# Performance work log

Measured on AMD Instinct MI355X. Metric: run time of the kernel, lower is better.

Reference implementation:

```python
import jax, jax.numpy as jnp
import numpy as np
from jax import lax

EPS = 1e-5
F_CH = 32  # TIM future channels = int(256/8)
B_CH = 32  # TIM past channels (note: source bug -> these are zeroed, not shifted)


def inorm(x):
    # InstanceNorm3d (no affine): normalize each (b, c) over (T, H, W), biased var
    m = jnp.mean(x, axis=(2, 3, 4), keepdims=True)
    v = jnp.var(x, axis=(2, 3, 4), keepdims=True)
    return (x - m) * lax.rsqrt(v + EPS)


def conv1x1(x, w):
    # pointwise conv: x [B,C,T,H,W], w [O,C]
    return jnp.einsum('bcthw,oc->bothw', x, w)


def dwconv(x, w, pad):
    # depthwise 3D conv; w [C,1,kd,kh,kw], pad = [(pd,pd),(ph,ph),(pw,pw)]
    return lax.conv_general_dilated(
        x, w, window_strides=(1, 1, 1), padding=pad,
        feature_group_count=x.shape[1],
        dimension_numbers=('NCDHW', 'OIDHW', 'NCDHW'))


def tim(x):
    # Non-circular temporal interlacing. Faithful to source (past slice is a no-op):
    # channels [0:f]  <- x shifted from future (t+1), zero-padded at last frame
    # channels [f:f+b] <- zeros
    # channels [f+b:] <- identity
    f, b = F_CH, B_CH
    fut = jnp.concatenate([x[:, :f, 1:], jnp.zeros_like(x[:, :f, :1])], axis=2)
    mid = jnp.zeros_like(x[:, f:f + b])
    return jnp.concatenate([fut, mid, x[:, f + b:]], axis=1)


def setup_inputs() -> dict:
    key = jax.random.key(0)
    ks = jax.random.split(key, 7)
    cin, hid, cout = 64, 256, 64
    x = jax.random.normal(ks[0], (4, cin, 16, 64, 64), dtype=jnp.float32)
    w1 = jax.random.normal(ks[1], (hid, cin), dtype=jnp.float32) * 0.05
    w_dw_s = jax.random.normal(ks[2], (hid, 1, 1, 3, 3), dtype=jnp.float32) * 0.1
    w_dw_t = jax.random.normal(ks[3], (hid, 1, 3, 1, 1), dtype=jnp.float32) * 0.1
    w_se1 = jax.random.normal(ks[4], (hid // 4, hid), dtype=jnp.float32) * 0.05
    w_se2 = jax.random.normal(ks[5], (hid, hid // 4), dtype=jnp.float32) * 0.05
    w_proj = jax.random.normal(ks[6], (cout, hid), dtype=jnp.float32) * 0.05
    return {'x': x, 'w1': w1, 'w_dw_s': w_dw_s, 'w_dw_t': w_dw_t,
            'w_se1': w_se1, 'w_se2': w_se2, 'w_proj': w_proj}


def reference(x, w1, w_dw_s, w_dw_t, w_se1, w_se2, w_proj):
    shortcut = x
    # stage1: expand 1x1 conv + IN + ReLU
    h = jax.nn.relu(inorm(conv1x1(x, w1)))
    # temporal interlace (zero-FLOP channel shift)
    h = tim(h)
    # stage2: depthwise spatial (1,3,3) + IN + ReLU
    h = jax.nn.relu(inorm(dwconv(h, w_dw_s, [(0, 0), (1, 1), (1, 1)])))
    # stage3: depthwise temporal (3,1,1) + IN + ReLU
    h = jax.nn.relu(inorm(dwconv(h, w_dw_t, [(1, 1), (0, 0), (0, 0)])))
    # squeeze-excite
    y = jnp.mean(h, axis=(2, 3, 4), keepdims=True)           # [B,C,1,1,1]
    y = jax.nn.relu(jnp.einsum('bcthw,oc->bothw', y, w_se1))
    y = jax.nn.sigmoid(jnp.einsum('bcthw,oc->bothw', y, w_se2))
    h = h * y
    # proj 1x1 + IN, residual, maxpool (1,2,2)
    out = inorm(conv1x1(h, w_proj)) + shortcut
    out = lax.reduce_window(out, -jnp.inf, lax.max,
                            (1, 1, 1, 2, 2), (1, 1, 1, 2, 2), 'VALID')
    return out
```

## Files before the change

kernel.cpp:

```cpp
#include <hip/hip_runtime.h>
#include <hip/hip_bf16.h>

#define B_   4
#define CIN  64
#define HID  256
#define COUT 64
#define T_   16
#define H_   64
#define W_   64
#define HW_  (H_*W_)
#define THW  (T_*HW_)
#define EPS  1e-5f

typedef unsigned short ushort_t;
typedef unsigned int   uint_t;
typedef short bf16x8 __attribute__((ext_vector_type(8)));
typedef float f32x4  __attribute__((ext_vector_type(4)));

#define SA1   0
#define SB1   1024
#define SM3   4096
#define SIS3  5120
#define SSES  6144
#define SAL   7168
#define SBE   8192
__device__ float g_stats[10240];
__device__ float g_eps [4*1024*256];
__device__ float g_epss[4*1024*256];
__device__ ushort_t g_wpack[32768];

__device__ __forceinline__ float bf2f(ushort_t u) {
    return __uint_as_float(((uint_t)u) << 16);
}
__device__ __forceinline__ ushort_t f2bf(float f) {
    uint_t u = __float_as_uint(f);
    uint_t r = u + 0x7fffu + ((u >> 16) & 1u);
    return (ushort_t)(r >> 16);
}
__device__ __forceinline__ void unpacknorm2(uint2 k, float a, float bb, float* v) {
    uint_t uu[2] = {k.x, k.y};
    #pragma unroll
    for (int j = 0; j < 2; ++j) {
        v[2*j]   = fmaxf(fmaf(__uint_as_float(uu[j] << 16),         a, bb), 0.f);
        v[2*j+1] = fmaxf(fmaf(__uint_as_float(uu[j] & 0xffff0000u), a, bb), 0.f);
    }
}

__global__ __launch_bounds__(256) void k_prep(const float* __restrict__ w1,
                                              const float* __restrict__ wproj) {
    int idx = blockIdx.x*256 + threadIdx.x;
    {
        int j = idx & 7, lane = (idx>>3) & 63, ot = (idx>>9) & 3;
        int ks = (idx>>11) & 1, wv = idx >> 12;
        int ln = lane & 15, q = lane >> 4;
        int o = wv*64 + ot*16 + ln, k = ks*32 + q*8 + j;
        g_wpack[idx] = f2bf(w1[o*CIN + k]);
    }
    {
        int j = idx & 7, lane = (idx>>3) & 63, ot = (idx>>9) & 3, kg = idx >> 11;
        int ln = lane & 15, q = lane >> 4;
        int o = ot*16 + ln, k = kg*32 + q*8 + j;
        g_wpack[16384 + idx] = f2bf(wproj[o*HID + k]);
    }
}

__global__ __launch_bounds__(256) void k_expand(const float* __restrict__ x,
                                                ushort_t* __restrict__ h1, int b0) {
    union SMem {
        ushort_t Bs[64*72];
        float    red[2][256][16];
    };
    __shared__ SMem sm;
    const int tid = threadIdx.x;
    const int bb  = blockIdx.y, gb = b0 + bb;
    const int pos0 = blockIdx.x * 64;
    const int lane = tid & 63, wv = tid >> 6;
    const int q = lane >> 4, ln = lane & 15;

    bf16x8 af[2][4];
    #pragma unroll
    for (int ks = 0; ks < 2; ++ks)
        #pragma unroll
        for (int ot = 0; ot < 4; ++ot)
            af[ks][ot] = *(const bf16x8*)&g_wpack[(((wv*2+ks)*4+ot)<<9) + lane*8];

    #pragma unroll
    for (int i = 0; i < 4; ++i) {
        int lin = i*1024 + tid*4;
        int k = lin >> 6, n0 = lin & 63;
        float4 v = *(const float4*)&x[(size_t)(gb*CIN + k) * THW + pos0 + n0];
        ushort_t* d = &sm.Bs[k*72 + ((n0 + 16*((k>>3)&3)) & 63)];
        d[0] = f2bf(v.x); d[1] = f2bf(v.y); d[2] = f2bf(v.z); d[3] = f2bf(v.w);
    }
    __syncthreads();

    f32x4 acc[4][4];
    #pragma unroll
    for (int i = 0; i < 4; ++i)
        #pragma unroll
        for (int j = 0; j < 4; ++j)
            acc[i][j] = (f32x4){0.f,0.f,0.f,0.f};

    #pragma unroll
    for (int ks = 0; ks < 2; ++ks) {
        bf16x8 bfr[4];
        #pragma unroll
        for (int nt = 0; nt < 4; ++nt) {
            union { short s[8]; bf16x8 v; } bu;
            #pragma unroll
            for (int j = 0; j < 8; ++j) {
                int k = ks*32 + q*8 + j;
                int nn = (nt*16 + ln + 16*((k>>3)&3)) & 63;
                bu.s[j] = (short)sm.Bs[k*72 + nn];
            }
            bfr[nt] = bu.v;
        }
        #pragma unroll
        for (int ot = 0; ot < 4; ++ot)
            #pragma unroll
            for (int nt = 0; nt < 4; ++nt)
                acc[ot][nt] = __builtin_amdgcn_mfma_f32_16x16x32_bf16(
                    af[ks][ot], bfr[nt], acc[ot][nt], 0, 0, 0);
    }

    float sp_[16], ssp_[16];
    #pragma unroll
    for (int i = 0; i < 16; ++i) { sp_[i] = 0.f; ssp_[i] = 0.f; }

    #pragma unroll
    for (int ot = 0; ot < 4; ++ot)
        #pragma unroll
        for (int nt = 0; nt < 4; ++nt)
            #pragma unroll
            for (int r = 0; r < 4; ++r) {
                float vv = acc[ot][nt][r];
                int o = wv*64 + ot*16 + q*4 + r;
                int n = nt*16 + ln;
                h1[((size_t)bb*HID + o)*THW + pos0 + n] = f2bf(vv);
                sp_[ot*4+r] += vv;
                ssp_[ot*4+r] = fmaf(vv, vv, ssp_[ot*4+r]);
            }

    __syncthreads();
    #pragma unroll
    for (int i = 0; i < 16; ++i) {
        int o = wv*64 + (i>>2)*16 + q*4 + (i&3);
        sm.red[0][o][ln] = sp_[i];
        sm.red[1][o][ln] = ssp_[i];
    }
    __syncthreads();
    {
        float s = 0.f, ss = 0.f;
        #pragma unroll
        for (int l = 0; l < 16; ++l) {
            s  += sm.red[0][tid][l];
            ss += sm.red[1][tid][l];
        }
        size_t base = ((size_t)bb*1024 + blockIdx.x)*256 + tid;
        g_eps [base] = s;
        g_epss[base] = ss;
    }
}

__global__ __launch_bounds__(256) void k_red() {
    const int tid = threadIdx.x;
    const int cg  = blockIdx.x;
    const int bb  = blockIdx.y;
    const int ch  = cg*16 + (tid & 15);
    const int pb0 = tid >> 4;
    const float* ps  = &g_eps [((size_t)bb*1024)*256];
    const float* pss = &g_epss[((size_t)bb*1024)*256];
    float s = 0.f, ss = 0.f;
    #pragma unroll 8
    for (int it = 0; it < 64; ++it) {
        int pb = it*16 + pb0;
        s  += ps [(size_t)pb*256 + ch];
        ss += pss[(size_t)pb*256 + ch];
    }
    __shared__ float rs[256], rss[256];
    rs[tid] = s; rss[tid] = ss;
    __syncthreads();
    if (tid < 16) {
        float st = 0.f, sst = 0.f;
        #pragma unroll
        for (int k = 0; k < 16; ++k) { st += rs[tid + 16*k]; sst += rss[tid + 16*k]; }
        float m = st * (1.f/THW);
        float v = sst * (1.f/THW) - m*m;
        float is = 1.f / sqrtf(v + EPS);
        int ch_ = cg*16 + tid;
        int bc = bb*HID + ch_;
        g_stats[SA1 + bc] = is;
        g_stats[SB1 + bc] = -m * is;
        if (ch_ >= 32 && ch_ < 64) {
            g_stats[SM3  + bc] = 0.f;
            g_stats[SIS3 + bc] = 1.f / sqrtf(EPS);
            g_stats[SSES + bc] = 0.f;
        }
    }
}

__global__ __launch_bounds__(1024) void k_mid(const ushort_t* __restrict__ h1,
                                              const float* __restrict__ wdws,
                                              const float* __restrict__ wdwt,
                                              ushort_t* __restrict__ h3) {
    const int tid = threadIdx.x;
    const int oc  = blockIdx.x;
    const int o   = (oc < 32) ? oc : oc + 32;
    const int bb  = blockIdx.y;
    const int bc  = bb*HID + o;
    const int wid = tid >> 6, lane = tid & 63;

    __shared__ float pl[4][66*67];
    __shared__ float ls[16], lss[16];
    __shared__ float sa, sb;

    const float a1 = g_stats[SA1 + bc];
    const float b1 = g_stats[SB1 + bc];

    if (tid < 66) {
        #pragma unroll
        for (int b = 0; b < 4; ++b) {
            pl[b][tid]         = 0.f;
            pl[b][65*67 + tid] = 0.f;
            pl[b][tid*67]      = 0.f;
            pl[b][tid*67 + 65] = 0.f;
        }
    }

    const int fut = (o < 32) ? 1 : 0;
    const int y   = tid >> 4;
    const int x0  = (tid & 15) * 4;
    const ushort_t* chp = h1 + (size_t)bc * THW;
    const int lastp = fut ? (T_-2) : (T_-1);

    float wf[9];
    #pragma unroll
    for (int k = 0; k < 9; ++k) wf[k] = wdws[o*9 + k];

    uint2 sreg[4];
    sreg[0] = *(const uint2*)(chp + (size_t)(0+fut)*HW_ + tid*4);
    sreg[1] = *(const uint2*)(chp + (size_t)(1+fut)*HW_ + tid*4);
    #pragma unroll
    for (int p = 0; p < 2; ++p) {
        float vv[4];
        unpacknorm2(sreg[p], a1, b1, vv);
        float* dst = &pl[p][(y+1)*67 + x0 + 1];
        #pragma unroll
        for (int i = 0; i < 4; ++i) dst[i] = vv[i];
    }
    sreg[2] = *(const uint2*)(chp + (size_t)(2+fut)*HW_ + tid*4);
    sreg[3] = *(const uint2*)(chp + (size_t)(3+fut)*HW_ + tid*4);
    __syncthreads();

    uint2 keep[16];
    float s2 = 0.f, ss2 = 0.f;

    #pragma unroll
    for (int it = 0; it < 8; ++it) {
        {
            int pA = 2*it + 4, pB = 2*it + 5;
            if (pA <= lastp)
                sreg[pA & 3] = *(const uint2*)(chp + (size_t)(pA+fut)*HW_ + tid*4);
            if (pB <= lastp)
                sreg[pB & 3] = *(const uint2*)(chp + (size_t)(pB+fut)*HW_ + tid*4);
        }
        #pragma unroll
        for (int w = 0; w < 2; ++w) {
            int wp = 2*it + 2 + w;
            if (wp <= lastp) {
                float vv[4];
                unpacknorm2(sreg[wp & 3], a1, b1, vv);
                float* dst = &pl[wp & 3][(y+1)*67 + x0 + 1];
                #pragma unroll
                for (int i = 0; i < 4; ++i) dst[i] = vv[i];
            }
        }
        #pragma unroll
        for (int cpi = 0; cpi < 2; ++cpi) {
            int t = 2*it + cpi;
            if (fut && t == T_-1) {
                keep[t] = (uint2){0u, 0u};
            } else {
                const float* plane = pl[t & 3];
                float v[3][6];
                #pragma unroll
                for (int dy = 0; dy < 3; ++dy) {
                    const float* rp = &plane[(y + dy)*67 + x0];
                    #pragma unroll
                    for (int j = 0; j < 6; ++j) v[dy][j] = rp[j];
                }
                uint_t outp[2];
                #pragma unroll
                for (int i2 = 0; i2 < 2; ++i2) {
                    float o0 = 0.f, o1 = 0.f;
                    #pragma unroll
                    for (int dy = 0; dy < 3; ++dy)
                        #pragma unroll
                        for (int dx = 0; dx < 3; ++dx) {
                            float w = wf[dy*3+dx];
                            o0 = fmaf(w, v[dy][2*i2 + dx],     o0);
                            o1 = fmaf(w, v[dy][2*i2 + 1 + dx], o1);
                        }
                    ushort_t u0 = f2bf(o0), u1 = f2bf(o1);
                    float r0 = bf2f(u0), r1 = bf2f(u1);
                    s2 += r0 + r1; ss2 = fmaf(r0, r0, fmaf(r1, r1, ss2));
                    outp[i2] = (uint_t)u0 | ((uint_t)u1 << 16);
                }
                keep[t].x = outp[0]; keep[t].y = outp[1];
            }
        }
        if (it < 7) __syncthreads();
    }

    {
        float s = s2, ss = ss2;
        #pragma unroll
        for (int m = 32; m > 0; m >>= 1) {
            s  += __shfl_xor(s,  m);
            ss += __shfl_xor(ss, m);
        }
        if (lane == 0) { ls[wid] = s; lss[wid] = ss; }
        __syncthreads();
        if (tid == 0) {
            float st = 0.f, sst = 0.f;
            #pragma unroll
            for (int i = 0; i < 16; ++i) { st += ls[i]; sst += lss[i]; }
            float m = st * (1.f/THW);
            float v = sst * (1.f/THW) - m*m;
            float is = 1.f / sqrtf(v + EPS);
            sa = is; sb = -m * is;
        }
        __syncthreads();
    }
    const float a2 = sa, b2 = sb;

    const float w0 = wdwt[o*3+0], w1 = wdwt[o*3+1], w2 = wdwt[o*3+2];
    ushort_t* op = h3 + (size_t)bc * THW + tid*4;

    float p[4], c[4], n[4];
    #pragma unroll
    for (int i = 0; i < 4; ++i) p[i] = 0.f;
    unpacknorm2(keep[0], a2, b2, c);
    unpacknorm2(keep[1], a2, b2, n);

    float s3 = 0.f, ss3 = 0.f;
    #pragma unroll
    for (int t = 0; t < T_; ++t) {
        uint_t outp[2];
        #pragma unroll
        for (int i2 = 0; i2 < 2; ++i2) {
            float o0 = fmaf(w0, p[2*i2],   fmaf(w1, c[2*i2],   w2 * n[2*i2]));
            float o1 = fmaf(w0, p[2*i2+1], fmaf(w1, c[2*i2+1], w2 * n[2*i2+1]));
            ushort_t u0 = f2bf(o0), u1 = f2bf(o1);
            float r0 = bf2f(u0), r1 = bf2f(u1);
            s3 += r0 + r1; ss3 = fmaf(r0, r0, fmaf(r1, r1, ss3));
            outp[i2] = (uint_t)u0 | ((uint_t)u1 << 16);
        }
        uint2 r; r.x = outp[0]; r.y = outp[1];
        *(uint2*)(op + (size_t)t*HW_) = r;

        #pragma unroll
        for (int i = 0; i < 4; ++i) { p[i] = c[i]; c[i] = n[i]; }
        if (t + 2 < T_) unpacknorm2(keep[t+2], a2, b2, n);
        else {
            #pragma unroll
            for (int i = 0; i < 4; ++i) n[i] = 0.f;
        }
        keep[t] = r;
    }

    {
        float s = s3, ss = ss3;
        #pragma unroll
        for (int m = 32; m > 0; m >>= 1) {
            s  += __shfl_xor(s,  m);
            ss += __shfl_xor(ss, m);
        }
        if (lane == 0) { ls[wid] = s; lss[wid] = ss; }
        __syncthreads();
        if (tid == 0) {
            float st = 0.f, sst = 0.f;
            #pragma unroll
            for (int i = 0; i < 16; ++i) { st += ls[i]; sst += lss[i]; }
            float m = st * (1.f/THW);
            float v = sst * (1.f/THW) - m*m;
            float is = 1.f / sqrtf(v + EPS);
            g_stats[SM3  + bc] = m;
            g_stats[SIS3 + bc] = is;
            sa = is; sb = -m * is;
        }
        __syncthreads();
    }

    const float a3 = sa, b3 = sb;
    float sse = 0.f;
    #pragma unroll
    for (int t = 0; t < T_; ++t) {
        uint_t uu[2] = {keep[t].x, keep[t].y};
        #pragma unroll
        for (int j = 0; j < 2; ++j) {
            sse += fmaxf(fmaf(__uint_as_float(uu[j] << 16),         a3, b3), 0.f);
            sse += fmaxf(fmaf(__uint_as_float(uu[j] & 0xffff0000u), a3, b3), 0.f);
        }
    }
    #pragma unroll
    for (int m = 32; m > 0; m >>= 1) sse += __shfl_xor(sse, m);
    if (lane == 0) ls[wid] = sse;
    __syncthreads();
    if (tid == 0) {
        float st = 0.f;
        #pragma unroll
        for (int i = 0; i < 16; ++i) st += ls[i];
        g_stats[SSES + bc] = st * (1.f/THW);
    }
}

__global__ __launch_bounds__(256) void k_semlp(const float* __restrict__ wse1,
                                               const float* __restrict__ wse2) {
    __shared__ float mv[HID];
    __shared__ float y1[64];
    const int bb = blockIdx.x, tid = threadIdx.x;
    mv[tid] = g_stats[SSES + bb*HID + tid];
    __syncthreads();
    if (tid < 64) {
        float acc = 0.f;
        #pragma unroll 8
        for (int c = 0; c < HID; ++c) acc = fmaf(wse1[tid*HID + c], mv[c], acc);
        y1[tid] = fmaxf(acc, 0.f);
    }
    __syncthreads();
    float z = 0.f;
    #pragma unroll
    for (int c = 0; c < 64; ++c) z = fmaf(wse2[tid*64 + c], y1[c], z);
    float se = 1.f / (1.f + expf(-z));
    const int bc = bb*HID + tid;
    float al = g_stats[SIS3 + bc] * se;
    if (tid >= 32 && tid < 64) al = 0.f;
    g_stats[SAL + bc] = al;
    g_stats[SBE + bc] = -g_stats[SM3 + bc] * al;
}

__global__ __launch_bounds__(256) void k_proj(const ushort_t* __restrict__ h3,
                                              float* __restrict__ proj) {
    __shared__ ushort_t Bs[64*136];
    const int tid = threadIdx.x;
    const int bb  = blockIdx.y;
    const int pos0 = blockIdx.x * 128;
    const int lane = tid & 63, wv = tid >> 6;
    const int q = lane >> 4, ln = lane & 15;

    f32x4 acc[4][2];
    #pragma unroll
    for (int i = 0; i < 4; ++i) {
        acc[i][0] = (f32x4){0.f,0.f,0.f,0.f};
        acc[i][1] = (f32x4){0.f,0.f,0.f,0.f};
    }

    for (int kc = 0; kc < 4; ++kc) {
        #pragma unroll
        for (int i = 0; i < 8; ++i) {
            int lin = i*1024 + tid*4;
            int kl = lin >> 7, n0 = lin & 127;
            int ch = bb*HID + kc*64 + kl;
            float al = g_stats[SAL + ch], be = g_stats[SBE + ch];
            ushort_t* d = &Bs[kl*136 + ((n0 + 16*((kl>>3)&7)) & 127)];
            if (al == 0.f) {
                d[0] = 0; d[1] = 0; d[2] = 0; d[3] = 0;
            } else {
                uint2 u = *(const uint2*)&h3[(size_t)ch * THW + pos0 + n0];
                float f0 = __uint_as_float(u.x << 16);
                float f1 = __uint_as_float(u.x & 0xffff0000u);
                float f2 = __uint_as_float(u.y << 16);
                float f3 = __uint_as_float(u.y & 0xffff0000u);
                d[0] = f2bf(fmaxf(fmaf(f0, al, be), 0.f));
                d[1] = f2bf(fmaxf(fmaf(f1, al, be), 0.f));
                d[2] = f2bf(fmaxf(fmaf(f2, al, be), 0.f));
                d[3] = f2bf(fmaxf(fmaf(f3, al, be), 0.f));
            }
        }
        __syncthreads();

        #pragma unroll
        for (int ks = 0; ks < 2; ++ks) {
            int kg = kc*2 + ks;
            bf16x8 af[4];
            #pragma unroll
            for (int ot = 0; ot < 4; ++ot)
                af[ot] = *(const bf16x8*)&g_wpack[16384 + ((kg*4+ot)<<9) + lane*8];
            bf16x8 bfr[2];
            #pragma unroll
            for (int nt = 0; nt < 2; ++nt) {
                union { short s[8]; bf16x8 v; } bu;
                #pragma unroll
                for (int j = 0; j < 8; ++j) {
                    int kl = ks*32 + q*8 + j;
                    int nn = (wv*32 + nt*16 + ln + 16*((kl>>3)&7)) & 127;
                    bu.s[j] = (short)Bs[kl*136 + nn];
                }
                bfr[nt] = bu.v;
            }
            #pragma unroll
            for (int ot = 0; ot < 4; ++ot)
                #pragma unroll
                for (int nt = 0; nt < 2; ++nt)
                    acc[ot][nt] = __builtin_amdgcn_mfma_f32_16x16x32_bf16(
                        af[ot], bfr[nt], acc[ot][nt], 0, 0, 0);
        }
        __syncthreads();
    }

    #pragma unroll
    for (int ot = 0; ot < 4; ++ot)
        #pragma unroll
        for (int nt = 0; nt < 2; ++nt)
            #pragma unroll
            for (int r = 0; r < 4; ++r) {
                int o = ot*16 + q*4 + r;
                int n = wv*32 + nt*16 + ln;
                proj[((size_t)bb*COUT + o)*THW + pos0 + n] = acc[ot][nt][r];
            }
}

__global__ __launch_bounds__(1024) void k_final(const float* __restrict__ proj,
                                                const float* __restrict__ x,
                                                float* __restrict__ out, int b0) {
    const int bo  = blockIdx.x;
    const int tid = threadIdx.x;
    const float* p = proj + (size_t)bo * THW;

    float s = 0.f, ss = 0.f;
    #pragma unroll
    for (int i = 0; i < THW/(1024*4); ++i) {
        float4 u = *(const float4*)(p + i*4096 + tid*4);
        s += u.x; ss = fmaf(u.x, u.x, ss);
        s += u.y; ss = fmaf(u.y, u.y, ss);
        s += u.z; ss = fmaf(u.z, u.z, ss);
        s += u.w; ss = fmaf(u.w, u.w, ss);
    }
    #pragma unroll
    for (int off = 32; off > 0; off >>= 1) {
        s  += __shfl_down(s,  off, 64);
        ss += __shfl_down(ss, off, 64);
    }
    __shared__ float ls[16], lss[16];
    __shared__ float sa, sb;
    int wid = tid >> 6, lane = tid & 63;
    if (lane == 0) { ls[wid] = s; lss[wid] = ss; }
    __syncthreads();
    if (tid == 0) {
        float st = 0.f, sst = 0.f;
        #pragma unroll
        for (int i = 0; i < 16; ++i) { st += ls[i]; sst += lss[i]; }
        float m = st * (1.f/THW);
        float v = sst * (1.f/THW) - m*m;
        float is = 1.f / sqrtf(v + EPS);
        sa = is; sb = -m * is;
    }
    __syncthreads();
    const float a = sa, bb = sb;

    const size_t gbase = (size_t)(b0*COUT + bo) * THW;
    float* op = out + (size_t)(b0*COUT + bo) * (T_*1024);
    #pragma unroll
    for (int i = 0; i < 16; ++i) {
        int idx = i*1024 + tid;
        int xx = idx & 31, yy = (idx >> 5) & 31, t = idx >> 10;
        float m = -3.4e38f;
        #pragma unroll
        for (int r = 0; r < 2; ++r) {
            size_t off = (size_t)t*HW_ + (size_t)(2*yy + r)*W_ + 2*xx;
            float2 p2 = *(const float2*)(p + off);
            float2 x2 = *(const float2*)(x + gbase + off);
            float v0 = fmaf(p2.x, a, bb) + x2.x;
            float v1 = fmaf(p2.y, a, bb) + x2.y;
            m = fmaxf(m, fmaxf(v0, v1));
        }
        op[idx] = m;
    }
}

extern "C" void kernel_launch(void* const* d_in, const int* in_sizes, int n_in,
                              void* d_out, int out_size, void* d_ws, size_t ws_size,
                              hipStream_t stream) {
    const float* x     = (const float*)d_in[0];
    const float* w1    = (const float*)d_in[1];
    const float* wdws  = (const float*)d_in[2];
    const float* wdwt  = (const float*)d_in[3];
    const float* wse1  = (const float*)d_in[4];
    const float* wse2  = (const float*)d_in[5];
    const float* wproj = (const float*)d_in[6];
    float* out = (float*)d_out;

    const size_t perb = 2ull * HID * THW * sizeof(ushort_t);
    int nb = (ws_size >= 4*perb) ? 4 : (ws_size >= 2*perb) ? 2 : 1;

    k_prep<<<64, 256, 0, stream>>>(w1, wproj);

    for (int b0 = 0; b0 < B_; b0 += nb) {
        char* ws = (char*)d_ws;
        ushort_t* h1   = (ushort_t*)ws;
        ushort_t* h3   = h1;
        float*    proj = (float*)(ws + (size_t)nb * HID*THW*2);

        k_expand<<<dim3(THW/64, nb), 256, 0, stream>>>(x, h1, b0);
        k_red   <<<dim3(16, nb), 256, 0, stream>>>();
        k_mid   <<<dim3(224, nb), 1024, 0, stream>>>(h1, wdws, wdwt, h3);
        k_semlp <<<nb, 256, 0, stream>>>(wse1, wse2);
        k_proj  <<<dim3(THW/128, nb), 256, 0, stream>>>(h3, proj);
        k_final <<<nb*COUT, 1024, 0, stream>>>(proj, x, out, b0);
    }
}
```

Measured before the change: 351.2 us.

## Store normalized h3 in k_mid and fold SE scale into per-batch proj weights

k_mid now applies the stage-3 instance norm and ReLU before writing h3 in bf16, so k_proj no longer has to normalize each element while staging it into shared memory. The squeeze-excite scale is folded into a per-batch copy of the projection weights built in k_semlp, and k_proj reads those scaled weights instead. This removes per-element FMA, max and bf16 conversion work from the GEMM staging loop. In exchange it adds a weight-repacking pass per batch and rounds to bf16 twice: once for the scaled weights and once for the normalized activations. The zeroed channels are no longer skipped in k_proj; they contribute zeros through the weights instead, which costs some extra global loads.

```diff
diff --git a/kernel.cpp b/kernel.cpp
--- a/kernel.cpp
+++ b/kernel.cpp
@@ -19,15 +19,12 @@
 
 #define SA1   0
 #define SB1   1024
-#define SM3   4096
-#define SIS3  5120
 #define SSES  6144
-#define SAL   7168
-#define SBE   8192
 __device__ float g_stats[10240];
 __device__ float g_eps [4*1024*256];
 __device__ float g_epss[4*1024*256];
 __device__ ushort_t g_wpack[32768];
+__device__ ushort_t g_wpackse[4*16384];
 
 __device__ __forceinline__ float bf2f(ushort_t u) {
     return __uint_as_float(((uint_t)u) << 16);
@@ -191,11 +188,8 @@
         int bc = bb*HID + ch_;
         g_stats[SA1 + bc] = is;
         g_stats[SB1 + bc] = -m * is;
-        if (ch_ >= 32 && ch_ < 64) {
-            g_stats[SM3  + bc] = 0.f;
-            g_stats[SIS3 + bc] = 1.f / sqrtf(EPS);
+        if (ch_ >= 32 && ch_ < 64)
             g_stats[SSES + bc] = 0.f;
-        }
     }
 }
 
@@ -335,7 +329,6 @@
     const float a2 = sa, b2 = sb;
 
     const float w0 = wdwt[o*3+0], w1 = wdwt[o*3+1], w2 = wdwt[o*3+2];
-    ushort_t* op = h3 + (size_t)bc * THW + tid*4;
 
     float p[4], c[4], n[4];
     #pragma unroll
@@ -357,7 +350,6 @@
             outp[i2] = (uint_t)u0 | ((uint_t)u1 << 16);
         }
         uint2 r; r.x = outp[0]; r.y = outp[1];
-        *(uint2*)(op + (size_t)t*HW_) = r;
 
         #pragma unroll
         for (int i = 0; i < 4; ++i) { p[i] = c[i]; c[i] = n[i]; }
@@ -385,23 +377,23 @@
             float m = st * (1.f/THW);
             float v = sst * (1.f/THW) - m*m;
             float is = 1.f / sqrtf(v + EPS);
-            g_stats[SM3  + bc] = m;
-            g_stats[SIS3 + bc] = is;
             sa = is; sb = -m * is;
         }
         __syncthreads();
     }
 
     const float a3 = sa, b3 = sb;
+    ushort_t* op = h3 + (size_t)bc * THW + tid*4;
     float sse = 0.f;
     #pragma unroll
     for (int t = 0; t < T_; ++t) {
-        uint_t uu[2] = {keep[t].x, keep[t].y};
-        #pragma unroll
-        for (int j = 0; j < 2; ++j) {
-            sse += fmaxf(fmaf(__uint_as_float(uu[j] << 16),         a3, b3), 0.f);
-            sse += fmaxf(fmaf(__uint_as_float(uu[j] & 0xffff0000u), a3, b3), 0.f);
-        }
+        float vv[4];
+        unpacknorm2(keep[t], a3, b3, vv);
+        sse += vv[0] + vv[1] + vv[2] + vv[3];
+        uint_t o0 = (uint_t)f2bf(vv[0]) | ((uint_t)f2bf(vv[1]) << 16);
+        uint_t o1 = (uint_t)f2bf(vv[2]) | ((uint_t)f2bf(vv[3]) << 16);
+        uint2 r; r.x = o0; r.y = o1;
+        *(uint2*)(op + (size_t)t*HW_) = r;
     }
     #pragma unroll
     for (int m = 32; m > 0; m >>= 1) sse += __shfl_xor(sse, m);
@@ -419,6 +411,7 @@
                                                const float* __restrict__ wse2) {
     __shared__ float mv[HID];
     __shared__ float y1[64];
+    __shared__ float sh_se[HID];
     const int bb = blockIdx.x, tid = threadIdx.x;
     mv[tid] = g_stats[SSES + bb*HID + tid];
     __syncthreads();
@@ -433,11 +426,15 @@
     #pragma unroll
     for (int c = 0; c < 64; ++c) z = fmaf(wse2[tid*64 + c], y1[c], z);
     float se = 1.f / (1.f + expf(-z));
-    const int bc = bb*HID + tid;
-    float al = g_stats[SIS3 + bc] * se;
-    if (tid >= 32 && tid < 64) al = 0.f;
-    g_stats[SAL + bc] = al;
-    g_stats[SBE + bc] = -g_stats[SM3 + bc] * al;
+    sh_se[tid] = (tid >= 32 && tid < 64) ? 0.f : se;
+    __syncthreads();
+    #pragma unroll 8
+    for (int i = 0; i < 64; ++i) {
+        int idx = i*256 + tid;
+        int j = idx & 7, lane = (idx>>3) & 63, kg = idx >> 11;
+        int k = kg*32 + (lane>>4)*8 + j;
+        g_wpackse[bb*16384 + idx] = f2bf(bf2f(g_wpack[16384 + idx]) * sh_se[k]);
+    }
 }
 
 __global__ __launch_bounds__(256) void k_proj(const ushort_t* __restrict__ h3,
@@ -462,21 +459,12 @@
             int lin = i*1024 + tid*4;
             int kl = lin >> 7, n0 = lin & 127;
             int ch = bb*HID + kc*64 + kl;
-            float al = g_stats[SAL + ch], be = g_stats[SBE + ch];
+            uint2 u = *(const uint2*)&h3[(size_t)ch * THW + pos0 + n0];
             ushort_t* d = &Bs[kl*136 + ((n0 + 16*((kl>>3)&7)) & 127)];
-            if (al == 0.f) {
-                d[0] = 0; d[1] = 0; d[2] = 0; d[3] = 0;
-            } else {
-                uint2 u = *(const uint2*)&h3[(size_t)ch * THW + pos0 + n0];
-                float f0 = __uint_as_float(u.x << 16);
-                float f1 = __uint_as_float(u.x & 0xffff0000u);
-                float f2 = __uint_as_float(u.y << 16);
-                float f3 = __uint_as_float(u.y & 0xffff0000u);
-                d[0] = f2bf(fmaxf(fmaf(f0, al, be), 0.f));
-                d[1] = f2bf(fmaxf(fmaf(f1, al, be), 0.f));
-                d[2] = f2bf(fmaxf(fmaf(f2, al, be), 0.f));
-                d[3] = f2bf(fmaxf(fmaf(f3, al, be), 0.f));
-            }
+            d[0] = (ushort_t)(u.x & 0xffffu);
+            d[1] = (ushort_t)(u.x >> 16);
+            d[2] = (ushort_t)(u.y & 0xffffu);
+            d[3] = (ushort_t)(u.y >> 16);
         }
         __syncthreads();
 
@@ -486,7 +474,7 @@
             bf16x8 af[4];
             #pragma unroll
             for (int ot = 0; ot < 4; ++ot)
-                af[ot] = *(const bf16x8*)&g_wpack[16384 + ((kg*4+ot)<<9) + lane*8];
+                af[ot] = *(const bf16x8*)&g_wpackse[bb*16384 + ((kg*4+ot)<<9) + lane*8];
             bf16x8 bfr[2];
             #pragma unroll
             for (int nt = 0; nt < 2; ++nt) {
```

Result: no change. 347.2 us (-1.1%).
